# Performance work log

Hardware: AMD Instinct MI355X
Metric: run time of the kernel (lower is better)

The kernel has to match this reference:

```python
import jax, jax.numpy as jnp
import numpy as np

B = 65536
HID = 512
NCLS = 10
NSUM = 19  # possible sums 0..18 of two digits


def _mlp(xi, W1, b1, W2, b2):
    # xi: [B, 28, 28] -> probs [B, 10]
    h = jax.nn.relu(xi.reshape(xi.shape[0], -1) @ W1 + b1)
    return jax.nn.softmax(h @ W2 + b2, axis=-1)


def setup_inputs() -> dict:
    key = jax.random.key(0)
    ks = jax.random.split(key, 9)
    s1 = 1.0 / np.sqrt(784.0)
    s2 = 1.0 / np.sqrt(float(HID))
    return {
        "x": jax.random.normal(ks[0], (2, B, 28, 28), dtype=jnp.float32),
        "W1_0": jax.random.normal(ks[1], (784, HID), dtype=jnp.float32) * s1,
        "b1_0": jnp.zeros((HID,), dtype=jnp.float32),
        "W2_0": jax.random.normal(ks[2], (HID, NCLS), dtype=jnp.float32) * s2,
        "b2_0": jnp.zeros((NCLS,), dtype=jnp.float32),
        "W1_1": jax.random.normal(ks[3], (784, HID), dtype=jnp.float32) * s1,
        "b1_1": jnp.zeros((HID,), dtype=jnp.float32),
        "W2_1": jax.random.normal(ks[4], (HID, NCLS), dtype=jnp.float32) * s2,
        "b2_1": jnp.zeros((NCLS,), dtype=jnp.float32),
    }


def reference(x, W1_0, b1_0, W2_0, b2_0, W1_1, b1_1, W2_1, b2_1):
    # per-network class probabilities
    p0 = _mlp(x[0], W1_0, b1_0, W2_0, b2_0)  # [B, 10]
    p1 = _mlp(x[1], W1_1, b1_1, W2_1, b2_1)  # [B, 10]

    # one-hot scatter matmuls + add == concat into the 20-literal labelling
    eye = jnp.eye(NCLS, dtype=p0.dtype)
    zer = jnp.zeros((NCLS, NCLS), dtype=p0.dtype)
    Wt0 = jnp.concatenate([eye, zer], axis=0)  # [20, 10]
    Wt1 = jnp.concatenate([zer, eye], axis=0)  # [20, 10]
    sdd_input = p0 @ Wt0.T + p1 @ Wt1.T       # [B, 20]

    lit0 = sdd_input[:, :NCLS]   # literals for digit 0
    lit1 = sdd_input[:, NCLS:]   # literals for digit 1

    # SDD evaluation with (add, mul): decision nodes sum prime*sub products.
    # Circuit semantics: P(sum=s) = sum_{a+c=s} lit0[a] * lit1[c]
    a = np.arange(NCLS)
    mask = (a[:, None] + a[None, :])[None, :, :] == np.arange(NSUM)[:, None, None]
    mask = jnp.asarray(mask, dtype=p0.dtype)  # [19, 10, 10]

    sdd_output = jnp.einsum('na,nc,sac->ns', lit0, lit1, mask)  # [B, 19]
    return sdd_output
```

## Files before the change

### kernel.cpp

```cpp
#include <hip/hip_runtime.h>
#include <hip/hip_fp16.h>

#define BATCH 65536
#define KDIM  784
#define HID   512
#define NTK   25
#define BM    64

typedef float    f32x4 __attribute__((ext_vector_type(4)));
typedef _Float16 f16x8 __attribute__((ext_vector_type(8)));
typedef _Float16 f16x4 __attribute__((ext_vector_type(4)));

__device__ __forceinline__ void gload_lds16(const void* g, void* l) {
  __builtin_amdgcn_global_load_lds((const __attribute__((address_space(1))) void*)g,
                                   (__attribute__((address_space(3))) void*)l, 16, 0, 0);
}

__global__ void prep_w1_kernel(const float* __restrict__ W1_0,
                               const float* __restrict__ W1_1,
                               _Float16* __restrict__ wsB) {
  int i = blockIdx.x * 256 + threadIdx.x;
  if (i >= 2 * 800 * 512) return;
  int net = i / (800 * 512);
  int rem = i - net * (800 * 512);
  int k = rem >> 9;
  int hid = rem & 511;
  const float* W = net ? W1_1 : W1_0;
  float v = (k < KDIM) ? W[k * 512 + hid] : 0.f;
  int kt = k >> 5, kk = k & 31;
  wsB[(((size_t)(net * NTK + kt) * HID + hid) << 5) + kk] = (_Float16)v;
}

__global__ void prep_w2_kernel(const float* __restrict__ W2_0,
                               const float* __restrict__ W2_1,
                               _Float16* __restrict__ wsW2) {
  int i = blockIdx.x * 256 + threadIdx.x;
  if (i >= 2 * 16 * 512) return;
  int net = i >> 13;
  int rem = i & 8191;
  int li = rem >> 9;
  int k = rem & 511;
  const float* W = net ? W2_1 : W2_0;
  wsW2[i] = (_Float16)((li < 10) ? W[k * 10 + li] : 0.f);
}

__launch_bounds__(256, 2)
__global__ void fused_mlp_kernel(const float* __restrict__ x,
                                 const float* __restrict__ b1_0,
                                 const float* __restrict__ b2_0,
                                 const float* __restrict__ b1_1,
                                 const float* __restrict__ b2_1,
                                 const _Float16* __restrict__ wsB,
                                 const _Float16* __restrict__ wsW2,
                                 float* __restrict__ out) {
  __shared__ __attribute__((aligned(16))) char hreg[65536];
  __shared__ float pbuf[2][BM * 17];

  const int t    = threadIdx.x;
  const int lane = t & 63;
  const int wid  = t >> 6;
  const int l15  = lane & 15;
  const int l4   = lane >> 4;
  const int hid0 = wid << 7;
  const int row0 = blockIdx.x * BM;

  const int sc0   = wid << 1;
  const int srowl = lane >> 3;
  const int sl7   = lane & 7;

  for (int net = 0; net < 2; ++net) {
    const float* xb = x + (size_t)net * BATCH * KDIM + (size_t)row0 * KDIM;
    const _Float16* wnet = wsB + (size_t)net * NTK * HID * 32;
    const float* b1 = net ? b1_1 : b1_0;
    const float* b2 = net ? b2_1 : b2_0;

    f32x4 acc[8][4];
#pragma unroll
    for (int rf = 0; rf < 8; ++rf)
#pragma unroll
      for (int nf = 0; nf < 4; ++nf) acc[rf][nf] = (f32x4){0.f, 0.f, 0.f, 0.f};

#pragma unroll
    for (int i = 0; i < 2; ++i) {
      int c = sc0 + i;
      int srow = (c << 3) + srowl;
      int kc = sl7 ^ (srow & 7);
      int kg = kc << 2;
      gload_lds16(xb + (size_t)srow * KDIM + kg, hreg + (c << 10));
    }
    __syncthreads();

    int bufb = 0;
    for (int kt = 0; kt < NTK; ++kt) {
      f16x8 bw[8];
      const _Float16* wk = wnet + ((size_t)kt * HID << 5);
#pragma unroll
      for (int rf = 0; rf < 8; ++rf)
        bw[rf] = *(const f16x8*)(wk + ((hid0 + (rf << 4) + l15) << 5) + (l4 << 3));

      if (kt < NTK - 1) {
#pragma unroll
        for (int i = 0; i < 2; ++i) {
          int c = sc0 + i;
          int srow = (c << 3) + srowl;
          int kc = sl7 ^ (srow & 7);
          int kg = ((kt + 1) << 5) + (kc << 2);
          if (kg >= KDIM) kg = 0;
          gload_lds16(xb + (size_t)srow * KDIM + kg, hreg + (bufb ^ 8192) + (c << 10));
        }
      }

      f16x8 bx[4];
#pragma unroll
      for (int nf = 0; nf < 4; ++nf) {
        int row = (nf << 4) + l15;
#pragma unroll
        for (int h = 0; h < 2; ++h) {
          int sl = ((l4 << 1) + h) ^ (row & 7);
          f32x4 v = *(const f32x4*)(hreg + bufb + (row << 7) + (sl << 4));
          bx[nf][h * 4 + 0] = (_Float16)v[0];
          bx[nf][h * 4 + 1] = (_Float16)v[1];
          bx[nf][h * 4 + 2] = (_Float16)v[2];
          bx[nf][h * 4 + 3] = (_Float16)v[3];
        }
      }

#pragma unroll
      for (int rf = 0; rf < 8; ++rf)
#pragma unroll
        for (int nf = 0; nf < 4; ++nf)
          acc[rf][nf] = __builtin_amdgcn_mfma_f32_16x16x32_f16(bw[rf], bx[nf], acc[rf][nf], 0, 0, 0);

      __syncthreads();
      bufb ^= 8192;
    }

#pragma unroll
    for (int rf = 0; rf < 8; ++rf) {
      f32x4 bv = *(const f32x4*)(b1 + hid0 + (rf << 4) + (l4 << 2));
#pragma unroll
      for (int nf = 0; nf < 4; ++nf) {
        f16x4 hv;
#pragma unroll
        for (int j = 0; j < 4; ++j)
          hv[j] = (_Float16)fmaxf(acc[rf][nf][j] + bv[j], 0.f);
        int row = (nf << 4) + l15;
        int slot = (wid << 4) + (rf << 1) + (l4 >> 1);
        *(f16x4*)(hreg + (row << 10) + ((slot ^ (row & 7)) << 4) + ((l4 & 1) << 3)) = hv;
      }
    }
    __syncthreads();

    f32x4 l2 = {0.f, 0.f, 0.f, 0.f};
    {
      const _Float16* w2n = wsW2 + (((net << 4) + l15) << 9);
      int row = (wid << 4) + l15;
#pragma unroll
      for (int kk = 0; kk < 16; ++kk) {
        f16x8 aw = *(const f16x8*)(w2n + (kk << 5) + (l4 << 3));
        int sl = ((kk << 2) + l4) ^ (row & 7);
        f16x8 bh = *(const f16x8*)(hreg + (row << 10) + (sl << 4));
        l2 = __builtin_amdgcn_mfma_f32_16x16x32_f16(aw, bh, l2, 0, 0, 0);
      }
    }

    int cls0 = l4 << 2;
    float lg[4];
#pragma unroll
    for (int j = 0; j < 4; ++j) {
      int c = cls0 + j;
      lg[j] = (c < 10) ? (l2[j] + b2[c]) : -1e30f;
    }
    float mx = fmaxf(fmaxf(lg[0], lg[1]), fmaxf(lg[2], lg[3]));
    mx = fmaxf(mx, __shfl_xor(mx, 16));
    mx = fmaxf(mx, __shfl_xor(mx, 32));
    float ev[4], s = 0.f;
#pragma unroll
    for (int j = 0; j < 4; ++j) {
      ev[j] = (cls0 + j < 10) ? __expf(lg[j] - mx) : 0.f;
      s += ev[j];
    }
    s += __shfl_xor(s, 16);
    s += __shfl_xor(s, 32);
    float inv = 1.f / s;
#pragma unroll
    for (int j = 0; j < 4; ++j) {
      int c = cls0 + j;
      if (c < 10) pbuf[net][((wid << 4) + l15) * 17 + c] = ev[j] * inv;
    }
    __syncthreads();
  }

  float* outb = (float*)hreg;
  {
    int r = t & 63;
    int sq = t >> 6;
#pragma unroll
    for (int si = 0; si < 5; ++si) {
      int s = sq * 5 + si;
      if (s < 19) {
        int alo = (s > 9) ? (s - 9) : 0;
        int ahi = (s < 9) ? s : 9;
        float a = 0.f;
        for (int aa = alo; aa <= ahi; ++aa)
          a += pbuf[0][r * 17 + aa] * pbuf[1][r * 17 + (s - aa)];
        outb[r * 19 + s] = a;
      }
    }
  }
  __syncthreads();
  {
    float* og = out + (size_t)row0 * 19;
    for (int i = t; i < BM * 19; i += 256) og[i] = outb[i];
  }
}

extern "C" void kernel_launch(void* const* d_in, const int* in_sizes, int n_in,
                              void* d_out, int out_size, void* d_ws, size_t ws_size,
                              hipStream_t stream) {
  (void)in_sizes; (void)n_in; (void)out_size; (void)ws_size;
  const float* x    = (const float*)d_in[0];
  const float* W1_0 = (const float*)d_in[1];
  const float* b1_0 = (const float*)d_in[2];
  const float* W2_0 = (const float*)d_in[3];
  const float* b2_0 = (const float*)d_in[4];
  const float* W1_1 = (const float*)d_in[5];
  const float* b1_1 = (const float*)d_in[6];
  const float* W2_1 = (const float*)d_in[7];
  const float* b2_1 = (const float*)d_in[8];
  float* out = (float*)d_out;

  _Float16* wsB  = (_Float16*)d_ws;
  _Float16* wsW2 = wsB + 2 * NTK * HID * 32;

  hipLaunchKernelGGL(prep_w1_kernel, dim3(3200), dim3(256), 0, stream, W1_0, W1_1, wsB);
  hipLaunchKernelGGL(prep_w2_kernel, dim3(64), dim3(256), 0, stream, W2_0, W2_1, wsW2);
  hipLaunchKernelGGL(fused_mlp_kernel, dim3(BATCH / BM), dim3(256), 0, stream,
                     x, b1_0, b2_0, b1_1, b2_1, wsB, wsW2, out);
}
```

Before: 231.3 us.

## Stage x in two large fp16 halves with 512-thread blocks instead of double-buffered K tiles

Replaces the per-K-tile double-buffered async global-to-LDS pipeline with two bulk phases. In each phase the block loads roughly half of each row's 784 features, converts them to fp16 once, and stores them in padded, swizzled LDS. The MMA loop then runs over 12 or 13 K tiles with no per-tile barrier. The block doubles to 512 threads (8 waves, 64 hidden units each) and the launch bound now targets 4 waves per SIMD with fewer accumulators, aiming to cut per-tile syncs and repeated fp32-to-fp16 conversion. The trade-off is that loads no longer overlap compute inside a block, so the design relies on occupancy across blocks to hide memory latency.

```diff
diff --git a/kernel.cpp b/kernel.cpp
--- a/kernel.cpp
+++ b/kernel.cpp
@@ -7,14 +7,12 @@
 #define NTK   25
 #define BM    64
 
+#define XSTRIDE 832
+#define HSTRIDE 1056
+
 typedef float    f32x4 __attribute__((ext_vector_type(4)));
 typedef _Float16 f16x8 __attribute__((ext_vector_type(8)));
 typedef _Float16 f16x4 __attribute__((ext_vector_type(4)));
-
-__device__ __forceinline__ void gload_lds16(const void* g, void* l) {
-  __builtin_amdgcn_global_load_lds((const __attribute__((address_space(1))) void*)g,
-                                   (__attribute__((address_space(3))) void*)l, 16, 0, 0);
-}
 
 __global__ void prep_w1_kernel(const float* __restrict__ W1_0,
                                const float* __restrict__ W1_1,
@@ -44,7 +42,7 @@
   wsW2[i] = (_Float16)((li < 10) ? W[k * 10 + li] : 0.f);
 }
 
-__launch_bounds__(256, 2)
+__launch_bounds__(512, 4)
 __global__ void fused_mlp_kernel(const float* __restrict__ x,
                                  const float* __restrict__ b1_0,
                                  const float* __restrict__ b2_0,
@@ -53,20 +51,16 @@
                                  const _Float16* __restrict__ wsB,
                                  const _Float16* __restrict__ wsW2,
                                  float* __restrict__ out) {
-  __shared__ __attribute__((aligned(16))) char hreg[65536];
-  __shared__ float pbuf[2][BM * 17];
+  __shared__ __attribute__((aligned(16))) char region[64 * HSTRIDE];
+  __shared__ float pbuf[2][BM * 11];
 
   const int t    = threadIdx.x;
   const int lane = t & 63;
   const int wid  = t >> 6;
   const int l15  = lane & 15;
   const int l4   = lane >> 4;
-  const int hid0 = wid << 7;
+  const int hid0 = wid << 6;
   const int row0 = blockIdx.x * BM;
-
-  const int sc0   = wid << 1;
-  const int srowl = lane >> 3;
-  const int sl7   = lane & 7;
 
   for (int net = 0; net < 2; ++net) {
     const float* xb = x + (size_t)net * BATCH * KDIM + (size_t)row0 * KDIM;
@@ -74,136 +68,156 @@
     const float* b1 = net ? b1_1 : b1_0;
     const float* b2 = net ? b2_1 : b2_0;
 
-    f32x4 acc[8][4];
-#pragma unroll
-    for (int rf = 0; rf < 8; ++rf)
+    f32x4 acc[4][4];
+#pragma unroll
+    for (int rf = 0; rf < 4; ++rf)
 #pragma unroll
       for (int nf = 0; nf < 4; ++nf) acc[rf][nf] = (f32x4){0.f, 0.f, 0.f, 0.f};
 
 #pragma unroll
-    for (int i = 0; i < 2; ++i) {
-      int c = sc0 + i;
-      int srow = (c << 3) + srowl;
-      int kc = sl7 ^ (srow & 7);
-      int kg = kc << 2;
-      gload_lds16(xb + (size_t)srow * KDIM + kg, hreg + (c << 10));
-    }
-    __syncthreads();
-
-    int bufb = 0;
-    for (int kt = 0; kt < NTK; ++kt) {
-      f16x8 bw[8];
-      const _Float16* wk = wnet + ((size_t)kt * HID << 5);
-#pragma unroll
-      for (int rf = 0; rf < 8; ++rf)
+    for (int it = 0; it < 12; ++it) {
+      int f = it * 512 + t;
+      int row = f / 96;
+      int kq = f - row * 96;
+      f32x4 v = *(const f32x4*)(xb + (size_t)row * KDIM + (kq << 2));
+      f16x4 hv;
+      hv[0] = (_Float16)v[0]; hv[1] = (_Float16)v[1];
+      hv[2] = (_Float16)v[2]; hv[3] = (_Float16)v[3];
+      int sp = (kq >> 1) ^ (row & 3);
+      *(f16x4*)(region + row * XSTRIDE + (sp << 4) + ((kq & 1) << 3)) = hv;
+    }
+    __syncthreads();
+    for (int ktl = 0; ktl < 12; ++ktl) {
+      const _Float16* wk = wnet + (((size_t)ktl * HID) << 5);
+      f16x8 bw[4], bx[4];
+#pragma unroll
+      for (int rf = 0; rf < 4; ++rf)
         bw[rf] = *(const f16x8*)(wk + ((hid0 + (rf << 4) + l15) << 5) + (l4 << 3));
-
-      if (kt < NTK - 1) {
-#pragma unroll
-        for (int i = 0; i < 2; ++i) {
-          int c = sc0 + i;
-          int srow = (c << 3) + srowl;
-          int kc = sl7 ^ (srow & 7);
-          int kg = ((kt + 1) << 5) + (kc << 2);
-          if (kg >= KDIM) kg = 0;
-          gload_lds16(xb + (size_t)srow * KDIM + kg, hreg + (bufb ^ 8192) + (c << 10));
-        }
-      }
-
-      f16x8 bx[4];
 #pragma unroll
       for (int nf = 0; nf < 4; ++nf) {
-        int row = (nf << 4) + l15;
-#pragma unroll
-        for (int h = 0; h < 2; ++h) {
-          int sl = ((l4 << 1) + h) ^ (row & 7);
-          f32x4 v = *(const f32x4*)(hreg + bufb + (row << 7) + (sl << 4));
-          bx[nf][h * 4 + 0] = (_Float16)v[0];
-          bx[nf][h * 4 + 1] = (_Float16)v[1];
-          bx[nf][h * 4 + 2] = (_Float16)v[2];
-          bx[nf][h * 4 + 3] = (_Float16)v[3];
-        }
-      }
-
-#pragma unroll
-      for (int rf = 0; rf < 8; ++rf)
+        int b = (nf << 4) + l15;
+        int sp = ((ktl << 2) + l4) ^ (b & 3);
+        bx[nf] = *(const f16x8*)(region + b * XSTRIDE + (sp << 4));
+      }
+#pragma unroll
+      for (int rf = 0; rf < 4; ++rf)
 #pragma unroll
         for (int nf = 0; nf < 4; ++nf)
           acc[rf][nf] = __builtin_amdgcn_mfma_f32_16x16x32_f16(bw[rf], bx[nf], acc[rf][nf], 0, 0, 0);
-
-      __syncthreads();
-      bufb ^= 8192;
-    }
-
-#pragma unroll
-    for (int rf = 0; rf < 8; ++rf) {
-      f32x4 bv = *(const f32x4*)(b1 + hid0 + (rf << 4) + (l4 << 2));
+    }
+    __syncthreads();
+
+#pragma unroll
+    for (int it = 0; it < 13; ++it) {
+      int f = it * 512 + t;
+      if (f < 6400) {
+        int row = f / 100;
+        int kq = f - row * 100;
+        f32x4 v = *(const f32x4*)(xb + (size_t)row * KDIM + 384 + (kq << 2));
+        f16x4 hv;
+        hv[0] = (_Float16)v[0]; hv[1] = (_Float16)v[1];
+        hv[2] = (_Float16)v[2]; hv[3] = (_Float16)v[3];
+        int sp = (kq >> 1) ^ (row & 3);
+        *(f16x4*)(region + row * XSTRIDE + (sp << 4) + ((kq & 1) << 3)) = hv;
+      }
+    }
+    if (t < 256) {
+      int row = t >> 2;
+      int kq = 100 + (t & 3);
+      int sp = (kq >> 1) ^ (row & 3);
+      *(f16x4*)(region + row * XSTRIDE + (sp << 4) + ((kq & 1) << 3)) =
+          (f16x4){(_Float16)0.f, (_Float16)0.f, (_Float16)0.f, (_Float16)0.f};
+    }
+    __syncthreads();
+    for (int ktl = 0; ktl < 13; ++ktl) {
+      const _Float16* wk = wnet + (((size_t)(12 + ktl) * HID) << 5);
+      f16x8 bw[4], bx[4];
+#pragma unroll
+      for (int rf = 0; rf < 4; ++rf)
+        bw[rf] = *(const f16x8*)(wk + ((hid0 + (rf << 4) + l15) << 5) + (l4 << 3));
+#pragma unroll
+      for (int nf = 0; nf < 4; ++nf) {
+        int b = (nf << 4) + l15;
+        int sp = ((ktl << 2) + l4) ^ (b & 3);
+        bx[nf] = *(const f16x8*)(region + b * XSTRIDE + (sp << 4));
+      }
+#pragma unroll
+      for (int rf = 0; rf < 4; ++rf)
+#pragma unroll
+        for (int nf = 0; nf < 4; ++nf)
+          acc[rf][nf] = __builtin_amdgcn_mfma_f32_16x16x32_f16(bw[rf], bx[nf], acc[rf][nf], 0, 0, 0);
+    }
+    __syncthreads();
+
+#pragma unroll
+    for (int rf = 0; rf < 4; ++rf) {
+      f32x4 b1v = *(const f32x4*)(b1 + hid0 + (rf << 4) + (l4 << 2));
 #pragma unroll
       for (int nf = 0; nf < 4; ++nf) {
         f16x4 hv;
 #pragma unroll
         for (int j = 0; j < 4; ++j)
-          hv[j] = (_Float16)fmaxf(acc[rf][nf][j] + bv[j], 0.f);
-        int row = (nf << 4) + l15;
-        int slot = (wid << 4) + (rf << 1) + (l4 >> 1);
-        *(f16x4*)(hreg + (row << 10) + ((slot ^ (row & 7)) << 4) + ((l4 & 1) << 3)) = hv;
-      }
-    }
-    __syncthreads();
-
-    f32x4 l2 = {0.f, 0.f, 0.f, 0.f};
-    {
+          hv[j] = (_Float16)fmaxf(acc[rf][nf][j] + b1v[j], 0.f);
+        int b = (nf << 4) + l15;
+        int hl = hid0 + (rf << 4) + (l4 << 2);
+        int sp = (hl >> 3) ^ (b & 3);
+        *(f16x4*)(region + b * HSTRIDE + (sp << 4) + ((hl & 4) << 1)) = hv;
+      }
+    }
+    __syncthreads();
+
+    if (wid < 4) {
+      f32x4 l2 = {0.f, 0.f, 0.f, 0.f};
       const _Float16* w2n = wsW2 + (((net << 4) + l15) << 9);
-      int row = (wid << 4) + l15;
+      int b = (wid << 4) + l15;
 #pragma unroll
       for (int kk = 0; kk < 16; ++kk) {
         f16x8 aw = *(const f16x8*)(w2n + (kk << 5) + (l4 << 3));
-        int sl = ((kk << 2) + l4) ^ (row & 7);
-        f16x8 bh = *(const f16x8*)(hreg + (row << 10) + (sl << 4));
+        int sp = ((kk << 2) + l4) ^ (b & 3);
+        f16x8 bh = *(const f16x8*)(region + b * HSTRIDE + (sp << 4));
         l2 = __builtin_amdgcn_mfma_f32_16x16x32_f16(aw, bh, l2, 0, 0, 0);
       }
-    }
-
-    int cls0 = l4 << 2;
-    float lg[4];
-#pragma unroll
-    for (int j = 0; j < 4; ++j) {
-      int c = cls0 + j;
-      lg[j] = (c < 10) ? (l2[j] + b2[c]) : -1e30f;
-    }
-    float mx = fmaxf(fmaxf(lg[0], lg[1]), fmaxf(lg[2], lg[3]));
-    mx = fmaxf(mx, __shfl_xor(mx, 16));
-    mx = fmaxf(mx, __shfl_xor(mx, 32));
-    float ev[4], s = 0.f;
-#pragma unroll
-    for (int j = 0; j < 4; ++j) {
-      ev[j] = (cls0 + j < 10) ? __expf(lg[j] - mx) : 0.f;
-      s += ev[j];
-    }
-    s += __shfl_xor(s, 16);
-    s += __shfl_xor(s, 32);
-    float inv = 1.f / s;
-#pragma unroll
-    for (int j = 0; j < 4; ++j) {
-      int c = cls0 + j;
-      if (c < 10) pbuf[net][((wid << 4) + l15) * 17 + c] = ev[j] * inv;
+      int cls0 = l4 << 2;
+      float lg[4];
+#pragma unroll
+      for (int j = 0; j < 4; ++j) {
+        int c = cls0 + j;
+        lg[j] = (c < 10) ? (l2[j] + b2[c]) : -1e30f;
+      }
+      float mx = fmaxf(fmaxf(lg[0], lg[1]), fmaxf(lg[2], lg[3]));
+      mx = fmaxf(mx, __shfl_xor(mx, 16));
+      mx = fmaxf(mx, __shfl_xor(mx, 32));
+      float ev[4], sum = 0.f;
+#pragma unroll
+      for (int j = 0; j < 4; ++j) {
+        ev[j] = (cls0 + j < 10) ? __expf(lg[j] - mx) : 0.f;
+        sum += ev[j];
+      }
+      sum += __shfl_xor(sum, 16);
+      sum += __shfl_xor(sum, 32);
+      float inv = 1.f / sum;
+#pragma unroll
+      for (int j = 0; j < 4; ++j) {
+        int c = cls0 + j;
+        if (c < 10) pbuf[net][b * 11 + c] = ev[j] * inv;
+      }
     }
     __syncthreads();
   }
 
-  float* outb = (float*)hreg;
+  float* outb = (float*)region;
   {
-    int r = t & 63;
-    int sq = t >> 6;
-#pragma unroll
-    for (int si = 0; si < 5; ++si) {
-      int s = sq * 5 + si;
+    int r = lane;
+    int sq = wid;
+#pragma unroll
+    for (int si = 0; si < 3; ++si) {
+      int s = sq * 3 + si;
       if (s < 19) {
         int alo = (s > 9) ? (s - 9) : 0;
         int ahi = (s < 9) ? s : 9;
         float a = 0.f;
         for (int aa = alo; aa <= ahi; ++aa)
-          a += pbuf[0][r * 17 + aa] * pbuf[1][r * 17 + (s - aa)];
+          a += pbuf[0][r * 11 + aa] * pbuf[1][r * 11 + (s - aa)];
         outb[r * 19 + s] = a;
       }
     }
@@ -211,7 +225,7 @@
   __syncthreads();
   {
     float* og = out + (size_t)row0 * 19;
-    for (int i = t; i < BM * 19; i += 256) og[i] = outb[i];
+    for (int i = t; i < BM * 19; i += 512) og[i] = outb[i];
   }
 }
 
@@ -235,6 +249,6 @@
 
   hipLaunchKernelGGL(prep_w1_kernel, dim3(3200), dim3(256), 0, stream, W1_0, W1_1, wsB);
   hipLaunchKernelGGL(prep_w2_kernel, dim3(64), dim3(256), 0, stream, W2_0, W2_1, wsW2);
-  hipLaunchKernelGGL(fused_mlp_kernel, dim3(BATCH / BM), dim3(256), 0, stream,
+  hipLaunchKernelGGL(fused_mlp_kernel, dim3(BATCH / BM), dim3(512), 0, stream,
                      x, b1_0, b2_0, b1_1, b2_1, wsB, wsW2, out);
 }
```

Result: slower. 491.2 us (+112.4%).
